# Optimization experiments

Hardware: AMD Instinct MI355X
Metric: run time of the kernel (lower is better)

## Reference

```python
import jax, jax.numpy as jnp
import numpy as np

B, H, W, NUM_CLASSES = 128, 224, 224, 1000
EPS = 1e-6


def setup_inputs() -> dict:
    key = jax.random.key(0)
    k1, k2, k3, k4, k5, k6 = jax.random.split(key, 6)
    # objects are probabilities fed straight to BCE -> keep strictly in (0,1)
    objects = jnp.clip(jax.random.uniform(k1, (B, H, W)), EPS, 1.0 - EPS)
    scores = jax.random.normal(k2, (B, NUM_CLASSES), dtype=jnp.float32)
    locs = jax.random.normal(k3, (B, 4, H, W), dtype=jnp.float32)
    label = jax.random.randint(k4, (B,), 0, NUM_CLASSES)
    obj_mask = (jax.random.uniform(k5, (B, H, W)) < 0.05).astype(jnp.float32)
    coords = jax.random.uniform(k6, (B, 4, H, W), dtype=jnp.float32)
    gt = jnp.concatenate([obj_mask[:, None], coords], axis=1)  # [B,5,H,W]
    return {
        "objects": objects,
        "scores": scores,
        "locs": locs,
        "label": label,
        "gt": gt,
        "obj_coor": jnp.float32(5.0),
        "no_obj_confi": jnp.float32(0.5),
        "img_class_weight": jnp.float32(1.0),
    }


def reference(objects, scores, locs, label, gt, obj_coor, no_obj_confi, img_class_weight):
    gt0 = gt[:, 0]                      # [B,H,W] objectness target in {0,1}
    obj_m = gt0 == 1.0
    noobj_m = gt0 == 0.0
    # BCE terms; clamp logs at -100 like torch's binary_cross_entropy
    log_p = jnp.maximum(jnp.log(objects), -100.0)
    log_1mp = jnp.maximum(jnp.log1p(-objects), -100.0)
    no_obj_confi_loss = jnp.sum(jnp.where(noobj_m, -log_1mp, 0.0))
    obj_confi_loss = jnp.sum(jnp.where(obj_m, -log_p, 0.0))
    # masked coordinate L2: sum over 4 coord channels at object cells
    sq = jnp.sum((locs - gt[:, 1:5]) ** 2, axis=1)  # [B,H,W]
    obj_coor_loss = jnp.sum(jnp.where(obj_m, sq, 0.0))
    # image-level classification: mean cross entropy
    logz = jax.nn.log_softmax(scores, axis=-1)
    img_class_loss = -jnp.mean(jnp.take_along_axis(logz, label[:, None], axis=1))
    batch_size = objects.shape[0]
    return img_class_weight * img_class_loss + (
        no_obj_confi * no_obj_confi_loss + obj_confi_loss + obj_coor * obj_coor_loss
    ) / batch_size
```

## Files before the change

### kernel.cpp

```cpp
#include <hip/hip_runtime.h>
#include <math.h>

#define HW4  12544
#define BATCH 128
#define NUM_CLASSES 1000
#define N4   (BATCH * HW4)
#define G    2
#define TPB  256
#define NTHREADS (N4 / G)
#define NBLOCKS  (NTHREADS / TPB)

typedef float v4f __attribute__((ext_vector_type(4)));


__launch_bounds__(TPB, 4)
__global__ void pixel_loss_kernel(const v4f* __restrict__ objects,
                                  const v4f* __restrict__ locs,
                                  const v4f* __restrict__ gt,
                                  const float* __restrict__ obj_coor_p,
                                  const float* __restrict__ no_obj_confi_p,
                                  float* __restrict__ ws) {
    const float coorW = *obj_coor_p;
    const float noW   = *no_obj_confi_p;

    const unsigned tid = blockIdx.x * TPB + threadIdx.x;

    v4f o[G], m4[G], gc[G][4], lc[G][4];
#pragma unroll
    for (int k = 0; k < G; ++k) {
        const unsigned g   = tid + (unsigned)(k * NTHREADS);
        const unsigned b   = g / HW4;
        const unsigned hw4 = g - b * HW4;
        const unsigned gtb = b * (5 * HW4) + hw4;
        const unsigned lcb = b * (4 * HW4) + hw4;

        o[k]  = objects[g];
        m4[k] = gt[gtb];
#pragma unroll
        for (int c = 0; c < 4; ++c) {
            gc[k][c] = gt[gtb + (unsigned)((1 + c) * HW4)];
            lc[k][c] = locs[lcb + (unsigned)(c * HW4)];
        }
    }

    asm volatile(""
        : "+v"(o[0]),     "+v"(o[1]),
          "+v"(m4[0]),    "+v"(m4[1]),
          "+v"(gc[0][0]), "+v"(gc[0][1]), "+v"(gc[0][2]), "+v"(gc[0][3]),
          "+v"(gc[1][0]), "+v"(gc[1][1]), "+v"(gc[1][2]), "+v"(gc[1][3]),
          "+v"(lc[0][0]), "+v"(lc[0][1]), "+v"(lc[0][2]), "+v"(lc[0][3]),
          "+v"(lc[1][0]), "+v"(lc[1][1]), "+v"(lc[1][2]), "+v"(lc[1][3]));

    float acc = 0.0f;
#pragma unroll
    for (int k = 0; k < G; ++k) {
        v4f sq = {0.f, 0.f, 0.f, 0.f};
#pragma unroll
        for (int c = 0; c < 4; ++c) {
            v4f d = lc[k][c] - gc[k][c];
            sq += d * d;
        }
#pragma unroll
        for (int j = 0; j < 4; ++j) {
            const float p = o[k][j];
            const float m = m4[k][j];
            const float lognop = fmaxf(__logf(1.0f - p), -100.0f);
            const float logp   = fmaxf(__logf(p), -100.0f);
            const float a = -noW * lognop;
            const float b = fmaf(coorW, sq[j], -logp);
            acc += fmaf(m, b - a, a);
        }
    }

#pragma unroll
    for (int off = 32; off > 0; off >>= 1)
        acc += __shfl_down(acc, off, 64);

    __shared__ float smem[4];
    const int lane = threadIdx.x & 63;
    const int wave = threadIdx.x >> 6;
    if (lane == 0) smem[wave] = acc;
    __syncthreads();
    if (threadIdx.x == 0) {
        atomicAdd(&ws[0], smem[0] + smem[1] + smem[2] + smem[3]);
    }
}

__global__ void class_loss_kernel(const float* __restrict__ scores,
                                  const int* __restrict__ label,
                                  float* __restrict__ ws) {
    const int b = blockIdx.x;
    const float* row = scores + b * NUM_CLASSES;

    __shared__ float red[4];
    __shared__ float s_bcast;
    const int lane = threadIdx.x & 63;
    const int wave = threadIdx.x >> 6;

    float mx = -INFINITY;
    for (int i = threadIdx.x; i < NUM_CLASSES; i += blockDim.x)
        mx = fmaxf(mx, row[i]);
#pragma unroll
    for (int off = 32; off > 0; off >>= 1)
        mx = fmaxf(mx, __shfl_down(mx, off, 64));
    if (lane == 0) red[wave] = mx;
    __syncthreads();
    if (threadIdx.x == 0)
        s_bcast = fmaxf(fmaxf(red[0], red[1]), fmaxf(red[2], red[3]));
    __syncthreads();
    mx = s_bcast;

    float se = 0.0f;
    for (int i = threadIdx.x; i < NUM_CLASSES; i += blockDim.x)
        se += __expf(row[i] - mx);
#pragma unroll
    for (int off = 32; off > 0; off >>= 1)
        se += __shfl_down(se, off, 64);
    __syncthreads();
    if (lane == 0) red[wave] = se;
    __syncthreads();
    if (threadIdx.x == 0) {
        float lse = mx + logf(red[0] + red[1] + red[2] + red[3]);
        atomicAdd(&ws[1], -(row[label[b]] - lse));
    }
}

__global__ void finalize_kernel(const float* __restrict__ ws,
                                const float* __restrict__ img_class_weight_p,
                                float* __restrict__ out) {
    if (threadIdx.x == 0 && blockIdx.x == 0) {
        float img_class_loss = ws[1] / (float)BATCH;
        out[0] = img_class_weight_p[0] * img_class_loss + ws[0] / (float)BATCH;
    }
}

extern "C" void kernel_launch(void* const* d_in, const int* in_sizes, int n_in,
                              void* d_out, int out_size, void* d_ws, size_t ws_size,
                              hipStream_t stream) {
    const float* objects = (const float*)d_in[0];
    const float* scores  = (const float*)d_in[1];
    const float* locs    = (const float*)d_in[2];
    const int*   label   = (const int*)d_in[3];
    const float* gt      = (const float*)d_in[4];
    const float* obj_coor         = (const float*)d_in[5];
    const float* no_obj_confi     = (const float*)d_in[6];
    const float* img_class_weight = (const float*)d_in[7];

    float* ws  = (float*)d_ws;
    float* out = (float*)d_out;

    hipMemsetAsync(ws, 0, 2 * sizeof(float), stream);

    pixel_loss_kernel<<<NBLOCKS, TPB, 0, stream>>>(
        (const v4f*)objects, (const v4f*)locs, (const v4f*)gt,
        obj_coor, no_obj_confi, ws);

    class_loss_kernel<<<BATCH, 256, 0, stream>>>(scores, label, ws);

    finalize_kernel<<<1, 64, 0, stream>>>(ws, img_class_weight, out);
}
```

Baseline: 282.3 us.

## Stage per-image pixel tiles into LDS via direct global-to-LDS loads

The pixel loss kernel now gives each block one contiguous 1024-pixel tile of a single image, so the batch index no longer has to be derived per element. All ten input streams are copied into shared memory with global_load_lds 16-byte transfers, after which threads read from LDS and compute the loss. The aim is to issue every global load up front without holding them in registers, keeping more memory requests in flight. In exchange the kernel uses 40KB of LDS per block, fewer blocks fit per CU, each thread handles 4 pixels instead of 8, and there is an extra barrier.

```diff
diff --git a/kernel.cpp b/kernel.cpp
--- a/kernel.cpp
+++ b/kernel.cpp
@@ -1,89 +1,93 @@
 #include <hip/hip_runtime.h>
 #include <math.h>
 
-#define HW4  12544
+#define HW    50176
 #define BATCH 128
 #define NUM_CLASSES 1000
-#define N4   (BATCH * HW4)
-#define G    2
-#define TPB  256
-#define NTHREADS (N4 / G)
-#define NBLOCKS  (NTHREADS / TPB)
+#define TPB   256
+#define TILE_PX        1024
+#define CHUNKS_PER_IMG 49
+#define NBLOCKS (BATCH * CHUNKS_PER_IMG)
+#define NSTREAMS 10
 
 typedef float v4f __attribute__((ext_vector_type(4)));
 
 
-__launch_bounds__(TPB, 4)
-__global__ void pixel_loss_kernel(const v4f* __restrict__ objects,
-                                  const v4f* __restrict__ locs,
-                                  const v4f* __restrict__ gt,
+__device__ __forceinline__ void load_lds16(const float* g, void* l) {
+    __builtin_amdgcn_global_load_lds(
+        (const __attribute__((address_space(1))) void*)g,
+        (__attribute__((address_space(3))) void*)l, 16, 0, 0);
+}
+
+__launch_bounds__(TPB, 2)
+__global__ void pixel_loss_kernel(const float* __restrict__ objects,
+                                  const float* __restrict__ locs,
+                                  const float* __restrict__ gt,
                                   const float* __restrict__ obj_coor_p,
                                   const float* __restrict__ no_obj_confi_p,
                                   float* __restrict__ ws) {
+    __shared__ v4f lds4[NSTREAMS * (TILE_PX / 4)];
+    char* lds = (char*)lds4;
+
     const float coorW = *obj_coor_p;
     const float noW   = *no_obj_confi_p;
 
-    const unsigned tid = blockIdx.x * TPB + threadIdx.x;
+    const unsigned b    = blockIdx.x / CHUNKS_PER_IMG;
+    const unsigned j    = blockIdx.x - b * CHUNKS_PER_IMG;
+    const unsigned pix0 = j * TILE_PX;
 
-    v4f o[G], m4[G], gc[G][4], lc[G][4];
+    const unsigned lane = threadIdx.x & 63;
+    const unsigned wave = threadIdx.x >> 6;
+
+    const float* g0 = objects + b * HW + pix0;
+    const float* gg = gt   + (unsigned)(b * 5 * HW) + pix0;
+    const float* gl = locs + (unsigned)(b * 4 * HW) + pix0;
+
+    const unsigned fo = wave * 256 + lane * 4;
+    char* lbase = lds + wave * 1024;
+
+    load_lds16(g0 + fo, lbase + 0 * 4096);
 #pragma unroll
-    for (int k = 0; k < G; ++k) {
-        const unsigned g   = tid + (unsigned)(k * NTHREADS);
-        const unsigned b   = g / HW4;
-        const unsigned hw4 = g - b * HW4;
-        const unsigned gtb = b * (5 * HW4) + hw4;
-        const unsigned lcb = b * (4 * HW4) + hw4;
+    for (int c = 0; c < 5; ++c)
+        load_lds16(gg + c * HW + fo, lbase + (1 + c) * 4096);
+#pragma unroll
+    for (int c = 0; c < 4; ++c)
+        load_lds16(gl + c * HW + fo, lbase + (6 + c) * 4096);
 
-        o[k]  = objects[g];
-        m4[k] = gt[gtb];
+    __syncthreads();
+
+    const unsigned t = threadIdx.x;
+    v4f o  = lds4[0 * 256 + t];
+    v4f m4 = lds4[1 * 256 + t];
+    v4f sq = {0.f, 0.f, 0.f, 0.f};
 #pragma unroll
-        for (int c = 0; c < 4; ++c) {
-            gc[k][c] = gt[gtb + (unsigned)((1 + c) * HW4)];
-            lc[k][c] = locs[lcb + (unsigned)(c * HW4)];
-        }
+    for (int c = 0; c < 4; ++c) {
+        v4f d = lds4[(6 + c) * 256 + t] - lds4[(2 + c) * 256 + t];
+        sq += d * d;
     }
-
-    asm volatile(""
-        : "+v"(o[0]),     "+v"(o[1]),
-          "+v"(m4[0]),    "+v"(m4[1]),
-          "+v"(gc[0][0]), "+v"(gc[0][1]), "+v"(gc[0][2]), "+v"(gc[0][3]),
-          "+v"(gc[1][0]), "+v"(gc[1][1]), "+v"(gc[1][2]), "+v"(gc[1][3]),
-          "+v"(lc[0][0]), "+v"(lc[0][1]), "+v"(lc[0][2]), "+v"(lc[0][3]),
-          "+v"(lc[1][0]), "+v"(lc[1][1]), "+v"(lc[1][2]), "+v"(lc[1][3]));
 
     float acc = 0.0f;
 #pragma unroll
-    for (int k = 0; k < G; ++k) {
-        v4f sq = {0.f, 0.f, 0.f, 0.f};
-#pragma unroll
-        for (int c = 0; c < 4; ++c) {
-            v4f d = lc[k][c] - gc[k][c];
-            sq += d * d;
-        }
-#pragma unroll
-        for (int j = 0; j < 4; ++j) {
-            const float p = o[k][j];
-            const float m = m4[k][j];
-            const float lognop = fmaxf(__logf(1.0f - p), -100.0f);
-            const float logp   = fmaxf(__logf(p), -100.0f);
-            const float a = -noW * lognop;
-            const float b = fmaf(coorW, sq[j], -logp);
-            acc += fmaf(m, b - a, a);
-        }
+    for (int k = 0; k < 4; ++k) {
+        const float p = o[k];
+        const float m = m4[k];
+        const float lognop = fmaxf(__logf(1.0f - p), -100.0f);
+        const float logp   = fmaxf(__logf(p), -100.0f);
+        const float a  = -noW * lognop;
+        const float bb = fmaf(coorW, sq[k], -logp);
+        acc += fmaf(m, bb - a, a);
     }
 
 #pragma unroll
     for (int off = 32; off > 0; off >>= 1)
         acc += __shfl_down(acc, off, 64);
 
-    __shared__ float smem[4];
-    const int lane = threadIdx.x & 63;
-    const int wave = threadIdx.x >> 6;
-    if (lane == 0) smem[wave] = acc;
     __syncthreads();
-    if (threadIdx.x == 0) {
-        atomicAdd(&ws[0], smem[0] + smem[1] + smem[2] + smem[3]);
-    }
+    float* lr = (float*)lds;
+    if (lane == 0) lr[wave] = acc;
+    __syncthreads();
+    if (threadIdx.x == 0)
+        atomicAdd(&ws[0], lr[0] + lr[1] + lr[2] + lr[3]);
 }
 
 __global__ void class_loss_kernel(const float* __restrict__ scores,
@@ -152,8 +156,7 @@
     hipMemsetAsync(ws, 0, 2 * sizeof(float), stream);
 
     pixel_loss_kernel<<<NBLOCKS, TPB, 0, stream>>>(
-        (const v4f*)objects, (const v4f*)locs, (const v4f*)gt,
-        obj_coor, no_obj_confi, ws);
+        objects, locs, gt, obj_coor, no_obj_confi, ws);
 
     class_loss_kernel<<<BATCH, 256, 0, stream>>>(scores, label, ws);
 
```

New measurement: 290.9 us. 3.0% more time.

## Skip coordinate loads for pixels with no positive objectness mask

Applied to the files above, without the earlier changes.

The pixel loss kernel now loads the four coordinate channels of locs and gt only when at least one of a thread's four objectness-mask values is positive. Since the coordinate term is multiplied by the mask, the result is unchanged. It also drops the two-elements-per-thread grouping, the asm register pinning and the occupancy hint from launch bounds, and launches one vector element per thread. The goal is to cut DRAM traffic on the eight coordinate streams. The risk is that the coordinate loads now wait on the mask load and are issued per lane under divergence. With a sparse but random mask, most cache lines may still be touched, so the traffic saving could be small.

```diff
diff --git a/kernel.cpp b/kernel.cpp
--- a/kernel.cpp
+++ b/kernel.cpp
@@ -1,19 +1,18 @@
 #include <hip/hip_runtime.h>
 #include <math.h>
 
-#define HW4  12544
+#define HW    50176
+#define HW4   12544
 #define BATCH 128
 #define NUM_CLASSES 1000
-#define N4   (BATCH * HW4)
-#define G    2
-#define TPB  256
-#define NTHREADS (N4 / G)
-#define NBLOCKS  (NTHREADS / TPB)
+#define N4    (BATCH * HW4)
+#define TPB   256
+#define NBLOCKS (N4 / TPB)
 
 typedef float v4f __attribute__((ext_vector_type(4)));
 
 
-__launch_bounds__(TPB, 4)
+__launch_bounds__(TPB)
 __global__ void pixel_loss_kernel(const v4f* __restrict__ objects,
                                   const v4f* __restrict__ locs,
                                   const v4f* __restrict__ gt,
@@ -23,53 +22,34 @@
     const float coorW = *obj_coor_p;
     const float noW   = *no_obj_confi_p;
 
-    const unsigned tid = blockIdx.x * TPB + threadIdx.x;
+    const unsigned g   = blockIdx.x * TPB + threadIdx.x;
+    const unsigned b   = g / HW4;
+    const unsigned hw4 = g - b * HW4;
+    const unsigned gtb = b * (5 * HW4) + hw4;
+    const unsigned lcb = b * (4 * HW4) + hw4;
 
-    v4f o[G], m4[G], gc[G][4], lc[G][4];
-#pragma unroll
-    for (int k = 0; k < G; ++k) {
-        const unsigned g   = tid + (unsigned)(k * NTHREADS);
-        const unsigned b   = g / HW4;
-        const unsigned hw4 = g - b * HW4;
-        const unsigned gtb = b * (5 * HW4) + hw4;
-        const unsigned lcb = b * (4 * HW4) + hw4;
-
-        o[k]  = objects[g];
-        m4[k] = gt[gtb];
-#pragma unroll
-        for (int c = 0; c < 4; ++c) {
-            gc[k][c] = gt[gtb + (unsigned)((1 + c) * HW4)];
-            lc[k][c] = locs[lcb + (unsigned)(c * HW4)];
-        }
-    }
-
-    asm volatile(""
-        : "+v"(o[0]),     "+v"(o[1]),
-          "+v"(m4[0]),    "+v"(m4[1]),
-          "+v"(gc[0][0]), "+v"(gc[0][1]), "+v"(gc[0][2]), "+v"(gc[0][3]),
-          "+v"(gc[1][0]), "+v"(gc[1][1]), "+v"(gc[1][2]), "+v"(gc[1][3]),
-          "+v"(lc[0][0]), "+v"(lc[0][1]), "+v"(lc[0][2]), "+v"(lc[0][3]),
-          "+v"(lc[1][0]), "+v"(lc[1][1]), "+v"(lc[1][2]), "+v"(lc[1][3]));
+    const v4f o  = objects[g];
+    const v4f m4 = gt[gtb];
 
     float acc = 0.0f;
 #pragma unroll
-    for (int k = 0; k < G; ++k) {
+    for (int j = 0; j < 4; ++j) {
+        const float p = o[j];
+        const float m = m4[j];
+        const float a  = -noW * fmaxf(__logf(1.0f - p), -100.0f);
+        const float nl = -fmaxf(__logf(p), -100.0f);
+        acc += fmaf(m, nl - a, a);
+    }
+
+    if (m4[0] + m4[1] + m4[2] + m4[3] > 0.0f) {
         v4f sq = {0.f, 0.f, 0.f, 0.f};
 #pragma unroll
         for (int c = 0; c < 4; ++c) {
-            v4f d = lc[k][c] - gc[k][c];
+            v4f d = locs[lcb + (unsigned)(c * HW4)] - gt[gtb + (unsigned)((1 + c) * HW4)];
             sq += d * d;
         }
-#pragma unroll
-        for (int j = 0; j < 4; ++j) {
-            const float p = o[k][j];
-            const float m = m4[k][j];
-            const float lognop = fmaxf(__logf(1.0f - p), -100.0f);
-            const float logp   = fmaxf(__logf(p), -100.0f);
-            const float a = -noW * lognop;
-            const float b = fmaf(coorW, sq[j], -logp);
-            acc += fmaf(m, b - a, a);
-        }
+        acc += coorW * (m4[0] * sq[0] + m4[1] * sq[1] +
+                        m4[2] * sq[2] + m4[3] * sq[3]);
     }
 
 #pragma unroll
@@ -81,9 +61,8 @@
     const int wave = threadIdx.x >> 6;
     if (lane == 0) smem[wave] = acc;
     __syncthreads();
-    if (threadIdx.x == 0) {
+    if (threadIdx.x == 0)
         atomicAdd(&ws[0], smem[0] + smem[1] + smem[2] + smem[3]);
-    }
 }
 
 __global__ void class_loss_kernel(const float* __restrict__ scores,
```

Measured after the change: 295.2 us. 4.5% more time.
